# Kernel tuning notes

Measured on AMD Instinct MI355X. Metric: run time of the kernel, lower is better.

The kernel has to match this reference:

```python
import jax, jax.numpy as jnp
import numpy as np

B, A, D = 32, 1024, 128
THR = 0.05  # proximity_threshold


def setup_inputs() -> dict:
    key = jax.random.key(0)
    k1, k2, k3, k4, k5 = jax.random.split(key, 5)
    s = 1.0 / np.sqrt(D)
    return {
        "agent_embeds": jax.random.normal(k1, (B, A, D), jnp.float32),
        "agent_coords": jax.random.uniform(k2, (B, A, 2), jnp.float32),
        "agent_mask": jax.random.randint(k3, (B, A), 0, 2).astype(jnp.int32),
        "W1": (jax.random.normal(k4, (D, D), jnp.float32) * s),
        "b1": jnp.zeros((D,), jnp.float32),
        "W2": (jax.random.normal(k5, (D, D), jnp.float32) * s),
        "b2": jnp.zeros((D,), jnp.float32),
    }


def _cluster(coords, valid):
    """Greedy sequential proximity clustering (same order/semantics as the torch loop).
    coords [A,2], valid [A] bool -> assigned [A] int32 (group id; invalid agents = -2)."""
    diff = coords[:, None, :] - coords[None, :, :]          # [A,A,2]
    near_all = jnp.sum(diff * diff, axis=-1) < (THR * THR)   # dist < thr  <=>  dist^2 < thr^2
    assigned0 = jnp.where(valid, -1, -2).astype(jnp.int32)

    def step(carry, i):
        assigned, gid = carry
        start = assigned[i] == -1                 # valid and not yet assigned -> new group
        take = start & near_all[i] & (assigned == -1)  # includes i (dist ii = 0)
        assigned = jnp.where(take, gid, assigned)
        gid = gid + start.astype(jnp.int32)
        return (assigned, gid), None

    (assigned, _), _ = jax.lax.scan(step, (assigned0, jnp.int32(0)), jnp.arange(A))
    return assigned


def reference(agent_embeds, agent_coords, agent_mask, W1, b1, W2, b2):
    valid = agent_mask.astype(bool)                          # [B,A]
    assigned = jax.vmap(_cluster)(agent_coords, valid)       # [B,A] int32

    w = valid.astype(agent_embeds.dtype)                     # [B,A]
    seg = jnp.where(valid, assigned, 0)                      # invalid -> seg 0 with weight 0

    def pool(emb, sg, wt):  # per batch: segment-mean into at most A groups (padded)
        sums = jax.ops.segment_sum(emb * wt[:, None], sg, num_segments=A)  # [A,D]
        cnt = jax.ops.segment_sum(wt, sg, num_segments=A)                  # [A]
        return sums / jnp.maximum(cnt, 1.0)[:, None], cnt > 0

    group_tokens, group_mask = jax.vmap(pool)(agent_embeds, seg, w)  # [B,A,D], [B,A]

    # group_proj MLP applied to the whole (zero-padded) token tensor, as in torch
    h = jax.nn.gelu(group_tokens @ W1 + b1, approximate=False)
    group_tokens = h @ W2 + b2

    agent_to_group = jnp.where(valid, assigned, -1)
    return group_tokens, group_mask, agent_to_group
```

## Files before the change

kernel.cpp:

```cpp
#include <hip/hip_runtime.h>
#include <hip/hip_bf16.h>

#define NB 32
#define NA 1024
#define ND 128
#define TG 16

__device__ __forceinline__ float gelu_exact(float x) {
    return 0.5f * x * (1.0f + erff(x * 0.7071067811865476f));
}

__device__ __forceinline__ float dist2(float ax, float ay, float bx, float by) {
    float dx = ax - bx, dy = ay - by;
    return __fadd_rn(__fmul_rn(dx, dx), __fmul_rn(dy, dy));
}

__global__ __launch_bounds__(1024, 1) void cluster_kernel(
    const float2* __restrict__ coords, const int* __restrict__ mask,
    int* __restrict__ assigned, int* __restrict__ gcount,
    float* __restrict__ sums, float* __restrict__ counts,
    float* __restrict__ out_mask, float* __restrict__ out_a2g,
    const float* __restrict__ b1, const float* __restrict__ W2,
    const float* __restrict__ b2, float* __restrict__ empty_row)
{
    __shared__ float2 ring[NA];
    __shared__ int done_s[16];
    __shared__ int lead_cnt;

    const int tid = threadIdx.x;

    if (blockIdx.x == NB) {
        float* hbuf = (float*)ring;
        if (tid < ND) hbuf[tid] = gelu_exact(b1[tid]);
        __syncthreads();
        if (tid < ND) {
            float acc = b2[tid];
            for (int k = 0; k < ND; ++k) acc += hbuf[k] * W2[k * ND + tid];
            empty_row[tid] = acc;
        }
        return;
    }

    const int b = blockIdx.x;
    const int w = tid >> 6;
    const int lane = tid & 63;

    if (tid < 16) done_s[tid] = -1;
    if (tid == 0) lead_cnt = 0;

    float2 p = coords[(b << 10) + tid];
    const bool valid = mask[(b << 10) + tid] != 0;
    int asg = valid ? -1 : -2;
    bool alive = valid;
    const float thr2 = 0.05f * 0.05f;

    __syncthreads();

    int seen = 0;
    int target = (w == 0) ? 0 : -1;

    while (true) {
        if (target < 0)
            target = __hip_atomic_load(&done_s[w - 1], __ATOMIC_ACQUIRE,
                                       __HIP_MEMORY_SCOPE_WORKGROUP);
        if (__ballot(alive) == 0ULL) {
            if (target >= 0) { seen = target; break; }
        } else {
            int c = __hip_atomic_load(&lead_cnt, __ATOMIC_ACQUIRE,
                                      __HIP_MEMORY_SCOPE_WORKGROUP);
            if (c > seen) {
                do {
                    float2 l = ring[seen];
                    float d2 = dist2(p.x, p.y, l.x, l.y);
                    if (alive && d2 < thr2) { asg = seen; alive = false; }
                    ++seen;
                } while (seen < c);
                continue;
            }
            if (target >= 0 && seen >= target) break;
        }
        __builtin_amdgcn_s_sleep(1);
    }

    __builtin_amdgcn_s_setprio(1);
    unsigned long long bal;
    while ((bal = __ballot(alive)) != 0ULL) {
        const int L = (int)__builtin_ctzll(bal);
        const float lx = __builtin_bit_cast(float,
            __builtin_amdgcn_readlane(__builtin_bit_cast(int, p.x), L));
        const float ly = __builtin_bit_cast(float,
            __builtin_amdgcn_readlane(__builtin_bit_cast(int, p.y), L));
        float d2 = dist2(p.x, p.y, lx, ly);
        bool take = alive && (d2 < thr2);
        if (take) { asg = seen; alive = false; }
        if (lane == 0) ring[seen] = make_float2(lx, ly);
        ++seen;
        if (lane == 0)
            __hip_atomic_store(&lead_cnt, seen, __ATOMIC_RELEASE,
                               __HIP_MEMORY_SCOPE_WORKGROUP);
    }
    if (lane == 0)
        __hip_atomic_store(&done_s[w], seen, __ATOMIC_RELEASE,
                           __HIP_MEMORY_SCOPE_WORKGROUP);
    __builtin_amdgcn_s_setprio(0);

    __syncthreads();
    const int G = lead_cnt;

    assigned[(b << 10) + tid] = asg;
    out_a2g[(b << 10) + tid] = (asg == -2) ? -1.0f : (float)asg;
    out_mask[(b << 10) + tid] = (tid < G) ? 1.0f : 0.0f;
    if (tid == 0) gcount[b] = G;

    const int Gpad = (G + TG - 1) & ~(TG - 1);
    float4* s4 = (float4*)(sums + (((size_t)b) << 10) * ND);
    for (int i = tid; i < Gpad * 32; i += 1024)
        s4[i] = make_float4(0.f, 0.f, 0.f, 0.f);
    if (tid < Gpad) counts[(b << 10) + tid] = 0.0f;
}

__global__ __launch_bounds__(256) void fill_kernel(
    const float* __restrict__ empty_row, float4* __restrict__ out0)
{
    const int idx = blockIdx.x * 256 + threadIdx.x;
    float4 r = ((const float4*)empty_row)[idx & 31];
    out0[idx] = r;
}

__global__ __launch_bounds__(256) void pool_kernel(
    const float4* __restrict__ emb, const int* __restrict__ assigned,
    float* __restrict__ sums, float* __restrict__ counts)
{
    const int idx = blockIdx.x * 256 + threadIdx.x;
    const int al = idx >> 5;
    const int dq = idx & 31;
    const int g = assigned[al];
    if (g < 0) return;
    const int b = al >> 10;
    float4 e = emb[(size_t)al * 32 + dq];
    float* s = sums + (((size_t)((b << 10) + g)) * ND) + dq * 4;
    atomicAdd(s + 0, e.x);
    atomicAdd(s + 1, e.y);
    atomicAdd(s + 2, e.z);
    atomicAdd(s + 3, e.w);
    if (dq == 0) atomicAdd(&counts[(b << 10) + g], 1.0f);
}

__global__ __launch_bounds__(256, 2) void mlp_kernel(
    const float* __restrict__ sums, const float* __restrict__ counts,
    const int* __restrict__ gcount,
    const float4* __restrict__ W1, const float* __restrict__ b1,
    const float4* __restrict__ W2, const float* __restrict__ b2,
    float* __restrict__ out0)
{
    const int b = blockIdx.y;
    const int g0 = blockIdx.x * TG;
    const int tid = threadIdx.x;
    if (g0 >= gcount[b]) return;
    float* ob = out0 + ((size_t)(b << 10) + g0) * ND;

    __shared__ float4 Wl[4096];
    __shared__ float tok[TG][ND];

    {
        const float4* s4 = (const float4*)(sums + ((size_t)(b << 10) + g0) * ND);
        float4* tdst = (float4*)&tok[0][0];
#pragma unroll
        for (int i = 0; i < 2; ++i) {
            int l = tid + i * 256;
            float c = fmaxf(counts[(b << 10) + g0 + (l >> 5)], 1.0f);
            float4 v = s4[l];
            tdst[l] = make_float4(v.x / c, v.y / c, v.z / c, v.w / c);
        }
    }
#pragma unroll
    for (int i = 0; i < 16; ++i) Wl[tid + i * 256] = W1[tid + i * 256];
    __syncthreads();

    const int jq = tid & 31;
    const int gs = tid >> 5;
    float acc[2][4];
#pragma unroll
    for (int jj = 0; jj < 4; ++jj) { acc[0][jj] = 0.0f; acc[1][jj] = 0.0f; }

#pragma unroll 4
    for (int dd = 0; dd < ND; ++dd) {
        float4 wv = Wl[dd * 32 + jq];
        float t0 = tok[gs][dd];
        float t1 = tok[gs + 8][dd];
        acc[0][0] += t0 * wv.x; acc[0][1] += t0 * wv.y;
        acc[0][2] += t0 * wv.z; acc[0][3] += t0 * wv.w;
        acc[1][0] += t1 * wv.x; acc[1][1] += t1 * wv.y;
        acc[1][2] += t1 * wv.z; acc[1][3] += t1 * wv.w;
    }
    float4 bb = ((const float4*)b1)[jq];
    __syncthreads();
    {
        float4 h;
        h.x = gelu_exact(acc[0][0] + bb.x);
        h.y = gelu_exact(acc[0][1] + bb.y);
        h.z = gelu_exact(acc[0][2] + bb.z);
        h.w = gelu_exact(acc[0][3] + bb.w);
        *(float4*)&tok[gs][jq * 4] = h;
        h.x = gelu_exact(acc[1][0] + bb.x);
        h.y = gelu_exact(acc[1][1] + bb.y);
        h.z = gelu_exact(acc[1][2] + bb.z);
        h.w = gelu_exact(acc[1][3] + bb.w);
        *(float4*)&tok[gs + 8][jq * 4] = h;
    }
#pragma unroll
    for (int i = 0; i < 16; ++i) Wl[tid + i * 256] = W2[tid + i * 256];
    __syncthreads();

#pragma unroll
    for (int jj = 0; jj < 4; ++jj) { acc[0][jj] = 0.0f; acc[1][jj] = 0.0f; }
#pragma unroll 4
    for (int dd = 0; dd < ND; ++dd) {
        float4 wv = Wl[dd * 32 + jq];
        float t0 = tok[gs][dd];
        float t1 = tok[gs + 8][dd];
        acc[0][0] += t0 * wv.x; acc[0][1] += t0 * wv.y;
        acc[0][2] += t0 * wv.z; acc[0][3] += t0 * wv.w;
        acc[1][0] += t1 * wv.x; acc[1][1] += t1 * wv.y;
        acc[1][2] += t1 * wv.z; acc[1][3] += t1 * wv.w;
    }
    float4 cbv = ((const float4*)b2)[jq];
    {
        float4 o;
        o.x = acc[0][0] + cbv.x; o.y = acc[0][1] + cbv.y;
        o.z = acc[0][2] + cbv.z; o.w = acc[0][3] + cbv.w;
        *(float4*)&ob[(size_t)gs * ND + jq * 4] = o;
        o.x = acc[1][0] + cbv.x; o.y = acc[1][1] + cbv.y;
        o.z = acc[1][2] + cbv.z; o.w = acc[1][3] + cbv.w;
        *(float4*)&ob[(size_t)(gs + 8) * ND + jq * 4] = o;
    }
}

extern "C" void kernel_launch(void* const* d_in, const int* in_sizes, int n_in,
                              void* d_out, int out_size, void* d_ws, size_t ws_size,
                              hipStream_t stream) {
    const float* emb    = (const float*)d_in[0];
    const float* coords = (const float*)d_in[1];
    const int*   mask   = (const int*)d_in[2];
    const float* W1     = (const float*)d_in[3];
    const float* b1     = (const float*)d_in[4];
    const float* W2     = (const float*)d_in[5];
    const float* b2     = (const float*)d_in[6];

    float* out0 = (float*)d_out;
    float* out1 = out0 + (size_t)NB * NA * ND;
    float* out2 = out1 + (size_t)NB * NA;

    float* ws_sums   = (float*)d_ws;
    float* ws_counts = ws_sums + (size_t)NB * NA * ND;
    int*   ws_asg    = (int*)(ws_counts + (size_t)NB * NA);
    int*   ws_gcnt   = ws_asg + (size_t)NB * NA;
    float* ws_empty  = (float*)(ws_gcnt + NB);

    cluster_kernel<<<NB + 1, 1024, 0, stream>>>(
        (const float2*)coords, mask, ws_asg, ws_gcnt,
        ws_sums, ws_counts, out1, out2,
        b1, W2, b2, ws_empty);
    fill_kernel<<<NB * NA * 32 / 256, 256, 0, stream>>>(
        ws_empty, (float4*)out0);
    pool_kernel<<<NB * NA * 32 / 256, 256, 0, stream>>>(
        (const float4*)emb, ws_asg, ws_sums, ws_counts);
    mlp_kernel<<<dim3(NA / TG, NB), 256, 0, stream>>>(
        ws_sums, ws_counts, ws_gcnt,
        (const float4*)W1, b1, (const float4*)W2, b2, out0);
}
```

Before: 170.9 us.

## Run greedy clustering in a single wavefront with register-resident agent slots

Replaces the 16-wave cross-wave ring-buffer clustering, which used LDS handoff and spin-waiting, with one 64-lane wavefront per batch. Each lane holds 16 agents in registers, and leaders are found with ballot/readlane and compared against the remaining slots. Zeroing of the sums and counts buffers moves from the cluster kernel into fill_kernel, which now zeros the whole buffer rather than only the used groups. This removes inter-wave synchronisation latency, but each leader now costs up to 16 distance checks per lane, and the fill kernel writes more memory.

```diff
diff --git a/kernel.cpp b/kernel.cpp
--- a/kernel.cpp
+++ b/kernel.cpp
@@ -15,116 +15,110 @@
     return __fadd_rn(__fmul_rn(dx, dx), __fmul_rn(dy, dy));
 }
 
-__global__ __launch_bounds__(1024, 1) void cluster_kernel(
+template <int S>
+__device__ __forceinline__ void proc_slot(const float2 (&cxy)[16], int (&asg)[16],
+                                          unsigned &m, int &gid, float thr2) {
+    unsigned long long cand;
+    while ((cand = __ballot((m >> S) & 1u)) != 0ULL) {
+        const int L = (int)__builtin_ctzll(cand);
+        const float lx = __builtin_bit_cast(float,
+            __builtin_amdgcn_readlane(__builtin_bit_cast(int, cxy[S].x), L));
+        const float ly = __builtin_bit_cast(float,
+            __builtin_amdgcn_readlane(__builtin_bit_cast(int, cxy[S].y), L));
+        unsigned take = 0u;
+#pragma unroll
+        for (int t = S; t < 16; ++t) {
+            const float d2 = dist2(cxy[t].x, cxy[t].y, lx, ly);
+            const bool tk = (d2 < thr2) && ((m >> t) & 1u);
+            if (tk) asg[t] = gid;
+            take |= (tk ? 1u : 0u) << t;
+        }
+        m &= ~take;
+        ++gid;
+    }
+}
+
+__global__ __launch_bounds__(64, 1) void cluster_kernel(
     const float2* __restrict__ coords, const int* __restrict__ mask,
     int* __restrict__ assigned, int* __restrict__ gcount,
-    float* __restrict__ sums, float* __restrict__ counts,
     float* __restrict__ out_mask, float* __restrict__ out_a2g,
     const float* __restrict__ b1, const float* __restrict__ W2,
     const float* __restrict__ b2, float* __restrict__ empty_row)
 {
-    __shared__ float2 ring[NA];
-    __shared__ int done_s[16];
-    __shared__ int lead_cnt;
-
-    const int tid = threadIdx.x;
+    const int lane = threadIdx.x;
 
     if (blockIdx.x == NB) {
-        float* hbuf = (float*)ring;
-        if (tid < ND) hbuf[tid] = gelu_exact(b1[tid]);
+        __shared__ float h0s[ND];
+        h0s[lane]      = gelu_exact(b1[lane]);
+        h0s[lane + 64] = gelu_exact(b1[lane + 64]);
         __syncthreads();
-        if (tid < ND) {
-            float acc = b2[tid];
-            for (int k = 0; k < ND; ++k) acc += hbuf[k] * W2[k * ND + tid];
-            empty_row[tid] = acc;
+        float a0 = b2[lane], a1 = b2[lane + 64];
+        for (int k = 0; k < ND; ++k) {
+            float h = h0s[k];
+            a0 += h * W2[k * ND + lane];
+            a1 += h * W2[k * ND + lane + 64];
         }
+        empty_row[lane]      = a0;
+        empty_row[lane + 64] = a1;
         return;
     }
 
     const int b = blockIdx.x;
-    const int w = tid >> 6;
-    const int lane = tid & 63;
-
-    if (tid < 16) done_s[tid] = -1;
-    if (tid == 0) lead_cnt = 0;
-
-    float2 p = coords[(b << 10) + tid];
-    const bool valid = mask[(b << 10) + tid] != 0;
-    int asg = valid ? -1 : -2;
-    bool alive = valid;
+    const float2* cb = coords + (b << 10);
+    const int*    mb = mask + (b << 10);
+
+    float2 cxy[16];
+    int asg[16];
+    unsigned m = 0;
+#pragma unroll
+    for (int s = 0; s < 16; ++s) {
+        cxy[s] = cb[s * 64 + lane];
+        int v = mb[s * 64 + lane];
+        asg[s] = v ? -1 : -2;
+        m |= (v ? 1u : 0u) << s;
+    }
+
     const float thr2 = 0.05f * 0.05f;
-
-    __syncthreads();
-
-    int seen = 0;
-    int target = (w == 0) ? 0 : -1;
-
-    while (true) {
-        if (target < 0)
-            target = __hip_atomic_load(&done_s[w - 1], __ATOMIC_ACQUIRE,
-                                       __HIP_MEMORY_SCOPE_WORKGROUP);
-        if (__ballot(alive) == 0ULL) {
-            if (target >= 0) { seen = target; break; }
-        } else {
-            int c = __hip_atomic_load(&lead_cnt, __ATOMIC_ACQUIRE,
-                                      __HIP_MEMORY_SCOPE_WORKGROUP);
-            if (c > seen) {
-                do {
-                    float2 l = ring[seen];
-                    float d2 = dist2(p.x, p.y, l.x, l.y);
-                    if (alive && d2 < thr2) { asg = seen; alive = false; }
-                    ++seen;
-                } while (seen < c);
-                continue;
-            }
-            if (target >= 0 && seen >= target) break;
-        }
-        __builtin_amdgcn_s_sleep(1);
-    }
-
-    __builtin_amdgcn_s_setprio(1);
-    unsigned long long bal;
-    while ((bal = __ballot(alive)) != 0ULL) {
-        const int L = (int)__builtin_ctzll(bal);
-        const float lx = __builtin_bit_cast(float,
-            __builtin_amdgcn_readlane(__builtin_bit_cast(int, p.x), L));
-        const float ly = __builtin_bit_cast(float,
-            __builtin_amdgcn_readlane(__builtin_bit_cast(int, p.y), L));
-        float d2 = dist2(p.x, p.y, lx, ly);
-        bool take = alive && (d2 < thr2);
-        if (take) { asg = seen; alive = false; }
-        if (lane == 0) ring[seen] = make_float2(lx, ly);
-        ++seen;
-        if (lane == 0)
-            __hip_atomic_store(&lead_cnt, seen, __ATOMIC_RELEASE,
-                               __HIP_MEMORY_SCOPE_WORKGROUP);
-    }
-    if (lane == 0)
-        __hip_atomic_store(&done_s[w], seen, __ATOMIC_RELEASE,
-                           __HIP_MEMORY_SCOPE_WORKGROUP);
-    __builtin_amdgcn_s_setprio(0);
-
-    __syncthreads();
-    const int G = lead_cnt;
-
-    assigned[(b << 10) + tid] = asg;
-    out_a2g[(b << 10) + tid] = (asg == -2) ? -1.0f : (float)asg;
-    out_mask[(b << 10) + tid] = (tid < G) ? 1.0f : 0.0f;
-    if (tid == 0) gcount[b] = G;
-
-    const int Gpad = (G + TG - 1) & ~(TG - 1);
-    float4* s4 = (float4*)(sums + (((size_t)b) << 10) * ND);
-    for (int i = tid; i < Gpad * 32; i += 1024)
-        s4[i] = make_float4(0.f, 0.f, 0.f, 0.f);
-    if (tid < Gpad) counts[(b << 10) + tid] = 0.0f;
+    int gid = 0;
+    proc_slot<0>(cxy, asg, m, gid, thr2);
+    proc_slot<1>(cxy, asg, m, gid, thr2);
+    proc_slot<2>(cxy, asg, m, gid, thr2);
+    proc_slot<3>(cxy, asg, m, gid, thr2);
+    proc_slot<4>(cxy, asg, m, gid, thr2);
+    proc_slot<5>(cxy, asg, m, gid, thr2);
+    proc_slot<6>(cxy, asg, m, gid, thr2);
+    proc_slot<7>(cxy, asg, m, gid, thr2);
+    proc_slot<8>(cxy, asg, m, gid, thr2);
+    proc_slot<9>(cxy, asg, m, gid, thr2);
+    proc_slot<10>(cxy, asg, m, gid, thr2);
+    proc_slot<11>(cxy, asg, m, gid, thr2);
+    proc_slot<12>(cxy, asg, m, gid, thr2);
+    proc_slot<13>(cxy, asg, m, gid, thr2);
+    proc_slot<14>(cxy, asg, m, gid, thr2);
+    proc_slot<15>(cxy, asg, m, gid, thr2);
+
+    int*   ab = assigned + (b << 10);
+    float* o2 = out_a2g + (b << 10);
+    float* o1 = out_mask + (b << 10);
+#pragma unroll
+    for (int s = 0; s < 16; ++s) {
+        int i = s * 64 + lane;
+        ab[i] = asg[s];
+        o2[i] = (asg[s] == -2) ? -1.0f : (float)asg[s];
+        o1[i] = (i < gid) ? 1.0f : 0.0f;
+    }
+    if (lane == 0) gcount[b] = gid;
 }
 
 __global__ __launch_bounds__(256) void fill_kernel(
-    const float* __restrict__ empty_row, float4* __restrict__ out0)
+    const float* __restrict__ empty_row, float4* __restrict__ out0,
+    float4* __restrict__ sums4, float* __restrict__ counts)
 {
     const int idx = blockIdx.x * 256 + threadIdx.x;
     float4 r = ((const float4*)empty_row)[idx & 31];
     out0[idx] = r;
+    sums4[idx] = make_float4(0.f, 0.f, 0.f, 0.f);
+    if (idx < NB * NA) counts[idx] = 0.0f;
 }
 
 __global__ __launch_bounds__(256) void pool_kernel(
@@ -257,12 +251,11 @@
     int*   ws_gcnt   = ws_asg + (size_t)NB * NA;
     float* ws_empty  = (float*)(ws_gcnt + NB);
 
-    cluster_kernel<<<NB + 1, 1024, 0, stream>>>(
+    cluster_kernel<<<NB + 1, 64, 0, stream>>>(
         (const float2*)coords, mask, ws_asg, ws_gcnt,
-        ws_sums, ws_counts, out1, out2,
-        b1, W2, b2, ws_empty);
+        out1, out2, b1, W2, b2, ws_empty);
     fill_kernel<<<NB * NA * 32 / 256, 256, 0, stream>>>(
-        ws_empty, (float4*)out0);
+        ws_empty, (float4*)out0, (float4*)ws_sums, ws_counts);
     pool_kernel<<<NB * NA * 32 / 256, 256, 0, stream>>>(
         (const float4*)emb, ws_asg, ws_sums, ws_counts);
     mlp_kernel<<<dim3(NA / TG, NB), 256, 0, stream>>>(
```

New measurement: 204.7 us. 19.8% more time.
